# Performance work log

Hardware: AMD Instinct MI355X
Metric: run time of the kernel (lower is better)

## Reference

```python
import jax, jax.numpy as jnp
import numpy as np

B, NA, NB, D, NH, APO = 32, 128, 128, 512, 16, 128
VA, VB, SUP_BDIST = 64, 32, 8
INV_SQRT_2PI_FACT = (2.0 * np.pi) ** 0.5


def setup_inputs() -> dict:
    key = jax.random.key(0)
    ks = jax.random.split(key, 20)
    atoms = jax.random.randint(ks[0], (B, NA), 0, VA)
    chirals = jax.random.randint(ks[1], (B, NA), 0, 4)
    coordinates = jax.random.normal(ks[2], (B, NA, 3), dtype=jnp.float32) * 5.0
    bonds = jax.random.randint(ks[3], (B, NA, NA), 0, VB)
    i0 = jax.random.randint(ks[4], (B, NB), 0, NA)
    off = jax.random.randint(ks[5], (B, NB), 1, NA)
    i1 = (i0 + off) % NA  # guarantee distinct endpoints so one-hot sum <= 1
    bond_indices = jnp.stack([i0, i1], axis=-1)
    bond_values = jax.random.randint(ks[6], (B, NB), 0, VB)
    bdist = jax.random.randint(ks[7], (B, NA, NA), 0, SUP_BDIST)
    sc = 0.02
    # embedding tables; rows for padding_idx=0 zeroed like torch nn.Embedding
    atype_emb = (jax.random.normal(ks[8], (VA, D)) * sc).at[0].set(0.0)
    chiral_emb = (jax.random.normal(ks[9], (4, D)) * sc).at[0].set(0.0)
    apair_w_tab = jax.random.normal(ks[10], (VA * VA, APO)) * sc
    apair_b_tab = jax.random.normal(ks[11], (VA * VA, APO)) * sc
    means = jax.random.normal(ks[12], (APO,)) * 0.1
    stds = jnp.ones((APO,), jnp.float32) + jax.random.normal(ks[13], (APO,)) * 0.1
    bond_emb_tab = (jax.random.normal(ks[14], (VB, NH)) * sc).at[0].set(0.0)
    lin_W = jax.random.normal(ks[15], (APO, NH)) * (1.0 / np.sqrt(APO))
    lin_b = jax.random.normal(ks[16], (NH,)) * sc
    btype_tab = (jax.random.normal(ks[17], (VB, D)) * sc).at[0].set(0.0)
    bond_atom_tab = (jax.random.normal(ks[18], (VA, D)) * sc).at[0].set(0.0)
    ab_connect_tab = (jax.random.normal(ks[19], (2, NH)) * sc).at[0].set(0.0)
    return dict(atoms=atoms, chirals=chirals, coordinates=coordinates, bonds=bonds,
                bond_indices=bond_indices, bond_values=bond_values, bdist=bdist,
                atype_emb=atype_emb, chiral_emb=chiral_emb, apair_w_tab=apair_w_tab,
                apair_b_tab=apair_b_tab, means=means, stds=stds, bond_emb_tab=bond_emb_tab,
                lin_W=lin_W, lin_b=lin_b, btype_tab=btype_tab, bond_atom_tab=bond_atom_tab,
                ab_connect_tab=ab_connect_tab)


def reference(atoms, chirals, coordinates, bonds, bond_indices, bond_values, bdist,
              atype_emb, chiral_emb, apair_w_tab, apair_b_tab, means, stds,
              bond_emb_tab, lin_W, lin_b, btype_tab, bond_atom_tab, ab_connect_tab):
    batch, n_atom = atoms.shape
    n_bond = bond_values.shape[1]
    # --- node embeddings ---
    atoms_e = atype_emb[atoms] + chiral_emb[chirals]                 # [B,Na,D]
    bonds_e = btype_tab[bond_values]                                  # [B,Nb,D]
    a0 = jnp.take_along_axis(atoms, bond_indices[:, :, 0], axis=1)    # [B,Nb]
    a1 = jnp.take_along_axis(atoms, bond_indices[:, :, 1], axis=1)
    bonds_e = bonds_e + bond_atom_tab[a0] + bond_atom_tab[a1]
    atoms_emb = jnp.concatenate([atoms_e, bonds_e], axis=1).transpose(1, 0, 2)  # [Na+Nb,B,D]
    # --- pairwise distances + RBF-modulated pair features ---
    diff = coordinates[:, None, :, :] - coordinates[:, :, None, :]    # [B,Na,Na,3]
    distances = jnp.sqrt(jnp.sum(diff * diff, axis=-1))               # [B,Na,Na]
    pair_idx = atoms[:, None, :] * VA + atoms[:, :, None]             # [B,Na,Na]
    x = apair_w_tab[pair_idx] * distances[..., None] + apair_b_tab[pair_idx]  # [B,Na,Na,APO]
    s = jnp.abs(stds) + 1e-5
    x = jnp.exp(-0.5 * jnp.square((x - means) / s)) / (INV_SQRT_2PI_FACT * s)
    apairs = jnp.einsum('bijp,ph->bijh', x, lin_W) + lin_b + bond_emb_tab[bonds]  # [B,Na,Na,NH]
    # --- atom-bond connectivity block ---
    oh = (jax.nn.one_hot(bond_indices[:, :, 0], n_atom, dtype=jnp.int32)
          + jax.nn.one_hot(bond_indices[:, :, 1], n_atom, dtype=jnp.int32))      # [B,Nb,Na]
    oh = oh * (bond_values != 0).astype(jnp.int32)[..., None]
    abpairs = ab_connect_tab[oh]                                       # [B,Nb,Na,NH]
    top = jnp.concatenate([apairs, abpairs], axis=1)                   # [B,Na+Nb,Na,NH]
    right = jnp.concatenate([abpairs.transpose(0, 2, 1, 3),
                             jnp.zeros((batch, n_bond, n_bond, NH), apairs.dtype)], axis=1)
    apairs = jnp.concatenate([top, right], axis=2)                     # [B,L,L,NH]
    padding_mask = jnp.concatenate([atoms == 0, bond_values == 0], axis=1)  # [B,L]
    apairs = jnp.where(padding_mask[:, None, :, None], -jnp.inf, apairs)
    apairs = apairs.transpose(0, 3, 1, 2)                              # [B,NH,L,L]
    # --- extended bdist ---
    oh_d = oh * SUP_BDIST
    bdist_out = jnp.concatenate([
        jnp.concatenate([bdist, oh_d], axis=1),
        jnp.concatenate([oh_d.transpose(0, 2, 1),
                         jnp.zeros((batch, n_bond, n_bond), oh_d.dtype)], axis=1)], axis=2)
    return atoms_emb, apairs, bdist_out, padding_mask
```

## Files before the change

kernel.cpp:

```cpp
#include <hip/hip_runtime.h>
#include <hip/hip_fp16.h>
#include <math.h>

#define B_ 32
#define NA_ 128
#define NB_ 128
#define D_ 512
#define NH_ 16
#define APO_ 128
#define L_ 256
#define VA_ 64

#define NEG_BIG (-3.0e38f)

#define WSB_WBT  2048
#define WSB_WBF  8192
#define WSB_BBF  (8192 + (1 << 20))
#define WS_NEED_BYTES (8192 + (2 << 20))

typedef __attribute__((ext_vector_type(8))) _Float16 f16x8;
typedef __attribute__((ext_vector_type(4))) float f32x4;

#define TROW 136

static __device__ __forceinline__ void nt_store(float* p, float v) {
    __builtin_nontemporal_store(v, p);
}
static __device__ __forceinline__ void nt_store2(float* p, float2 v) {
    __builtin_nontemporal_store(v.x, p);
    __builtin_nontemporal_store(v.y, p + 1);
}

__global__ __launch_bounds__(256) void k0_fold(
    const float* __restrict__ wtab, const float* __restrict__ btab,
    const float* __restrict__ means, const float* __restrict__ stds,
    const float* __restrict__ linW, char* __restrict__ wsb) {
    int t = blockIdx.x * 256 + threadIdx.x;
    int ai = t >> 13;
    int aj = (t >> 7) & 63;
    int p = t & (APO_ - 1);
    int src = (aj << 13) + (ai << 7) + p;
    float s = fabsf(stds[p]) + 1e-5f;
    float si = 1.0f / s;
    _Float16* wbf = (_Float16*)(wsb + WSB_WBF);
    _Float16* bbf = (_Float16*)(wsb + WSB_BBF);
    wbf[t] = (_Float16)(wtab[src] * si);
    bbf[t] = (_Float16)((btab[src] - means[p]) * si);
    if (blockIdx.x == 0) {
        _Float16* wbT = (_Float16*)(wsb + WSB_WBT);
        for (int q = threadIdx.x; q < NH_ * APO_; q += 256) {
            int h = q >> 7, pp = q & 127;
            float s2 = fabsf(stds[pp]) + 1e-5f;
            float cof = 0.39894228040143270f / s2;
            wbT[q] = (_Float16)(linW[pp * NH_ + h] * cof);
        }
    }
}

__global__ __launch_bounds__(256, 4) void k_mega(
    const int* __restrict__ atoms, const int* __restrict__ chirals,
    const float* __restrict__ coords, const int* __restrict__ bonds,
    const int* __restrict__ bond_idx, const int* __restrict__ bond_vals,
    const int* __restrict__ bdist,
    const float* __restrict__ atype, const float* __restrict__ chiral_t,
    const float* __restrict__ btype, const float* __restrict__ batom,
    const float* __restrict__ ab_tab, const float* __restrict__ linb,
    const float* __restrict__ bond_emb, const char* __restrict__ wsb,
    float* __restrict__ out0, float* __restrict__ out1,
    float* __restrict__ out2, float* __restrict__ out3) {
    __shared__ _Float16 tab[2][64 * TROW];
    float (*epi)[129] = (float (*)[129]) & tab[0][0];

    int b = blockIdx.x >> 8;
    int r = blockIdx.x & 255;
    int tid = threadIdx.x;

    if (r < NA_) {
        int i = r;
        int wave = tid >> 6;
        int lane = tid & 63;
        int col = lane & 15;
        int kg = lane >> 4;

        int ai = atoms[b * NA_ + i];

        const _Float16* gw = (const _Float16*)(wsb + WSB_WBF) + (size_t)ai * (64 * APO_);
        const _Float16* gb = (const _Float16*)(wsb + WSB_BBF) + (size_t)ai * (64 * APO_);
#pragma unroll
        for (int it = 0; it < 4; ++it) {
            int g = (it * 256 + tid) * 8;
            int row = g >> 7, off = g & 127;
            *(f16x8*)&tab[0][row * TROW + off] = *(const f16x8*)(gw + g);
            *(f16x8*)&tab[1][row * TROW + off] = *(const f16x8*)(gb + g);
        }

        int j2 = tid & 127;
        int hg = tid >> 7;
        int ajr2 = atoms[b * NA_ + j2];
        int bij2 = bonds[((size_t)b * NA_ + i) * NA_ + j2];
        const float4* ber4 = (const float4*)(bond_emb + (size_t)bij2 * NH_);
        float4 berA = ber4[hg * 2 + 0];
        float4 berB = ber4[hg * 2 + 1];

        float cx = coords[((size_t)b * NA_ + i) * 3 + 0];
        float cy = coords[((size_t)b * NA_ + i) * 3 + 1];
        float cz = coords[((size_t)b * NA_ + i) * 3 + 2];
        __half2 d2[2];
        int rowh[2];
#pragma unroll
        for (int tt = 0; tt < 2; ++tt) {
            int jA = (wave * 2 + tt) * 16 + col;
            int ajt = atoms[b * NA_ + jA];
            float dx = coords[((size_t)b * NA_ + jA) * 3 + 0] - cx;
            float dy = coords[((size_t)b * NA_ + jA) * 3 + 1] - cy;
            float dz = coords[((size_t)b * NA_ + jA) * 3 + 2] - cz;
            float dist = sqrtf(dx * dx + dy * dy + dz * dz);
            d2[tt] = __float2half2_rn(dist);
            rowh[tt] = ajt * TROW;
        }

        const _Float16* wbT = (const _Float16*)(wsb + WSB_WBT);
        f16x8 Bf[4];
#pragma unroll
        for (int ks = 0; ks < 4; ++ks)
            Bf[ks] = *(const f16x8*)(wbT + col * APO_ + ks * 32 + kg * 8);

        const __half2 KE2 = __float2half2_rn(-0.72134752044448170f);

        __syncthreads();

        f32x4 accv[2];
#pragma unroll
        for (int tt = 0; tt < 2; ++tt) {
            f32x4 acc = {0.f, 0.f, 0.f, 0.f};
#pragma unroll
            for (int ks = 0; ks < 4; ++ks) {
                f16x8 w8 = *(const f16x8*)&tab[0][rowh[tt] + ks * 32 + kg * 8];
                f16x8 b8 = *(const f16x8*)&tab[1][rowh[tt] + ks * 32 + kg * 8];
                const __half2* wh = (const __half2*)&w8;
                const __half2* bh = (const __half2*)&b8;
                f16x8 af;
                __half2* eh = (__half2*)&af;
#pragma unroll
                for (int q = 0; q < 4; ++q) {
                    __half2 xh = __hfma2(wh[q], d2[tt], bh[q]);
                    __half2 t2 = __hmul2(__hmul2(xh, xh), KE2);
                    eh[q] = h2exp2(t2);
                }
                acc = __builtin_amdgcn_mfma_f32_16x16x32_f16(af, Bf[ks], acc, 0, 0, 0);
            }
            accv[tt] = acc;
        }
        __syncthreads();

#pragma unroll
        for (int tt = 0; tt < 2; ++tt) {
            int jb = (wave * 2 + tt) * 16;
#pragma unroll
            for (int rr = 0; rr < 4; ++rr)
                epi[col][jb + kg * 4 + rr] = accv[tt][rr];
        }
        __syncthreads();

        float berx[8] = {berA.x, berA.y, berA.z, berA.w, berB.x, berB.y, berB.z, berB.w};
        bool maskj = (ajr2 == 0);
        float* opb = out1 + (size_t)b * NH_ * L_ * L_ + (size_t)(hg * 8) * (L_ * L_)
                   + (size_t)i * L_ + j2;
#pragma unroll
        for (int q = 0; q < 8; ++q) {
            int h = hg * 8 + q;
            float v = epi[h][j2] + linb[h] + berx[q];
            nt_store(opb + (size_t)q * (L_ * L_), maskj ? NEG_BIG : v);
        }
    }

    int c = tid;

    {
        float2 v;
        if (r < NA_) {
            int a = atoms[b * NA_ + r];
            int ch = chirals[b * NA_ + r];
            float2 v1 = ((const float2*)(atype + (size_t)a * D_))[c];
            float2 v2 = ((const float2*)(chiral_t + (size_t)ch * D_))[c];
            v = make_float2(v1.x + v2.x, v1.y + v2.y);
        } else {
            int k = r - NA_;
            int bv = bond_vals[b * NB_ + k];
            int i0 = bond_idx[(b * NB_ + k) * 2 + 0];
            int i1 = bond_idx[(b * NB_ + k) * 2 + 1];
            int a0 = atoms[b * NA_ + i0];
            int a1 = atoms[b * NA_ + i1];
            float2 v1 = ((const float2*)(btype + (size_t)bv * D_))[c];
            float2 v2 = ((const float2*)(batom + (size_t)a0 * D_))[c];
            float2 v3 = ((const float2*)(batom + (size_t)a1 * D_))[c];
            v = make_float2(v1.x + v2.x + v3.x, v1.y + v2.y + v3.y);
        }
        nt_store2(out0 + ((size_t)r * B_ + b) * D_ + 2 * c, v);
    }

    {
        float v = 0.0f;
        if (r < NA_) {
            if (c < NA_) {
                v = (float)bdist[((size_t)b * NA_ + r) * NA_ + c];
            } else {
                int k = c - NA_;
                int bv = bond_vals[b * NB_ + k];
                int i0 = bond_idx[(b * NB_ + k) * 2 + 0];
                int i1 = bond_idx[(b * NB_ + k) * 2 + 1];
                v = (bv != 0 && (i0 == r || i1 == r)) ? 8.0f : 0.0f;
            }
        } else if (c < NA_) {
            int k = r - NA_;
            int bv = bond_vals[b * NB_ + k];
            int i0 = bond_idx[(b * NB_ + k) * 2 + 0];
            int i1 = bond_idx[(b * NB_ + k) * 2 + 1];
            v = (bv != 0 && (i0 == c || i1 == c)) ? 8.0f : 0.0f;
        }
        nt_store(out2 + ((size_t)b * L_ + r) * L_ + c, v);
    }

    if (r == 0) {
        bool m = (c < NA_) ? (atoms[b * NA_ + c] == 0)
                           : (bond_vals[b * NB_ + (c - NA_)] == 0);
        nt_store(out3 + b * L_ + c, m ? 1.0f : 0.0f);
    }

    if (r >= NA_ || c >= NA_) {
        float ohv = 0.0f;
        bool mask;
        if (c < NA_) {
            int k = r - NA_;
            int bv = bond_vals[b * NB_ + k];
            int i0 = bond_idx[(b * NB_ + k) * 2 + 0];
            int i1 = bond_idx[(b * NB_ + k) * 2 + 1];
            ohv = (bv != 0 && (i0 == c || i1 == c)) ? 1.0f : 0.0f;
            mask = (atoms[b * NA_ + c] == 0);
        } else {
            int k = c - NA_;
            int bv = bond_vals[b * NB_ + k];
            mask = (bv == 0);
            if (r < NA_) {
                int i0 = bond_idx[(b * NB_ + k) * 2 + 0];
                int i1 = bond_idx[(b * NB_ + k) * 2 + 1];
                ohv = (bv != 0 && (i0 == r || i1 == r)) ? 1.0f : 0.0f;
            }
        }
        float* op = out1 + (size_t)b * NH_ * L_ * L_ + (size_t)r * L_ + c;
#pragma unroll
        for (int h = 0; h < NH_; ++h) {
            float v = mask ? NEG_BIG : ohv * ab_tab[NH_ + h];
            nt_store(op + (size_t)h * (L_ * L_), v);
        }
    }
}

__global__ __launch_bounds__(128) void k2_pair(
    const int* __restrict__ atoms, const float* __restrict__ coords,
    const int* __restrict__ bonds, const float* __restrict__ wtab,
    const float* __restrict__ btab, const float* __restrict__ linW,
    const float* __restrict__ linb, const float* __restrict__ bond_emb,
    const float* __restrict__ means, const float* __restrict__ stds,
    float* __restrict__ out1) {
    int b = blockIdx.x >> 7;
    int i = blockIdx.x & (NA_ - 1);
    int j = threadIdx.x;
    int ai = atoms[b * NA_ + i];
    int aj = atoms[b * NA_ + j];
    float cx = coords[((size_t)b * NA_ + i) * 3 + 0];
    float cy = coords[((size_t)b * NA_ + i) * 3 + 1];
    float cz = coords[((size_t)b * NA_ + i) * 3 + 2];
    float dx = coords[((size_t)b * NA_ + j) * 3 + 0] - cx;
    float dy = coords[((size_t)b * NA_ + j) * 3 + 1] - cy;
    float dz = coords[((size_t)b * NA_ + j) * 3 + 2] - cz;
    float dist = sqrtf(dx * dx + dy * dy + dz * dz);
    int idx = aj * VA_ + ai;
    const float4* wrow = (const float4*)(wtab + (size_t)idx * APO_);
    const float4* brow = (const float4*)(btab + (size_t)idx * APO_);
    float acc[NH_];
#pragma unroll
    for (int h = 0; h < NH_; ++h) acc[h] = 0.0f;
    const float KE = -0.72134752044448170f;
    for (int pp = 0; pp < APO_ / 4; ++pp) {
        float4 w4 = wrow[pp];
        float4 b4 = brow[pp];
        const float* wq = (const float*)&w4;
        const float* bq = (const float*)&b4;
#pragma unroll
        for (int q = 0; q < 4; ++q) {
            int p = pp * 4 + q;
            float s = fabsf(stds[p]) + 1e-5f;
            float si = 1.0f / s;
            float xh = fmaf(wq[q] * si, dist, fmaf(bq[q], si, -means[p] * si));
            float g = si * 0.39894228040143270f * exp2f(KE * xh * xh);
            const float* Wr = linW + p * NH_;
#pragma unroll
            for (int h = 0; h < NH_; ++h) acc[h] = fmaf(g, Wr[h], acc[h]);
        }
    }
    int bij = bonds[((size_t)b * NA_ + i) * NA_ + j];
    bool maskj = (aj == 0);
    float* op = out1 + (size_t)b * NH_ * L_ * L_ + (size_t)i * L_ + j;
#pragma unroll
    for (int h = 0; h < NH_; ++h) {
        float v = acc[h] + linb[h] + bond_emb[(size_t)bij * NH_ + h];
        op[(size_t)h * (L_ * L_)] = maskj ? NEG_BIG : v;
    }
}

__global__ __launch_bounds__(256) void k_fill(
    const int* __restrict__ atoms, const int* __restrict__ chirals,
    const int* __restrict__ bond_idx, const int* __restrict__ bond_vals,
    const int* __restrict__ bdist,
    const float* __restrict__ atype, const float* __restrict__ chiral_t,
    const float* __restrict__ btype, const float* __restrict__ batom,
    const float* __restrict__ ab_tab,
    float* __restrict__ out0, float* __restrict__ out1,
    float* __restrict__ out2, float* __restrict__ out3) {
    int b = blockIdx.x >> 8;
    int r = blockIdx.x & 255;
    int c = threadIdx.x;
    {
        float2 v;
        if (r < NA_) {
            int a = atoms[b * NA_ + r];
            int ch = chirals[b * NA_ + r];
            float2 v1 = ((const float2*)(atype + (size_t)a * D_))[c];
            float2 v2 = ((const float2*)(chiral_t + (size_t)ch * D_))[c];
            v = make_float2(v1.x + v2.x, v1.y + v2.y);
        } else {
            int k = r - NA_;
            int bv = bond_vals[b * NB_ + k];
            int i0 = bond_idx[(b * NB_ + k) * 2 + 0];
            int i1 = bond_idx[(b * NB_ + k) * 2 + 1];
            int a0 = atoms[b * NA_ + i0];
            int a1 = atoms[b * NA_ + i1];
            float2 v1 = ((const float2*)(btype + (size_t)bv * D_))[c];
            float2 v2 = ((const float2*)(batom + (size_t)a0 * D_))[c];
            float2 v3 = ((const float2*)(batom + (size_t)a1 * D_))[c];
            v = make_float2(v1.x + v2.x + v3.x, v1.y + v2.y + v3.y);
        }
        ((float2*)(out0 + ((size_t)r * B_ + b) * D_))[c] = v;
    }
    {
        float v = 0.0f;
        if (r < NA_) {
            if (c < NA_) {
                v = (float)bdist[((size_t)b * NA_ + r) * NA_ + c];
            } else {
                int k = c - NA_;
                int bv = bond_vals[b * NB_ + k];
                int i0 = bond_idx[(b * NB_ + k) * 2 + 0];
                int i1 = bond_idx[(b * NB_ + k) * 2 + 1];
                v = (bv != 0 && (i0 == r || i1 == r)) ? 8.0f : 0.0f;
            }
        } else if (c < NA_) {
            int k = r - NA_;
            int bv = bond_vals[b * NB_ + k];
            int i0 = bond_idx[(b * NB_ + k) * 2 + 0];
            int i1 = bond_idx[(b * NB_ + k) * 2 + 1];
            v = (bv != 0 && (i0 == c || i1 == c)) ? 8.0f : 0.0f;
        }
        out2[((size_t)b * L_ + r) * L_ + c] = v;
    }
    if (r == 0) {
        bool m = (c < NA_) ? (atoms[b * NA_ + c] == 0)
                           : (bond_vals[b * NB_ + (c - NA_)] == 0);
        out3[b * L_ + c] = m ? 1.0f : 0.0f;
    }
    if (r >= NA_ || c >= NA_) {
        float ohv = 0.0f;
        bool mask;
        if (c < NA_) {
            int k = r - NA_;
            int bv = bond_vals[b * NB_ + k];
            int i0 = bond_idx[(b * NB_ + k) * 2 + 0];
            int i1 = bond_idx[(b * NB_ + k) * 2 + 1];
            ohv = (bv != 0 && (i0 == c || i1 == c)) ? 1.0f : 0.0f;
            mask = (atoms[b * NA_ + c] == 0);
        } else {
            int k = c - NA_;
            int bv = bond_vals[b * NB_ + k];
            mask = (bv == 0);
            if (r < NA_) {
                int i0 = bond_idx[(b * NB_ + k) * 2 + 0];
                int i1 = bond_idx[(b * NB_ + k) * 2 + 1];
                ohv = (bv != 0 && (i0 == r || i1 == r)) ? 1.0f : 0.0f;
            }
        }
        float* op = out1 + (size_t)b * NH_ * L_ * L_ + (size_t)r * L_ + c;
#pragma unroll
        for (int h = 0; h < NH_; ++h) {
            float v = mask ? NEG_BIG : ohv * ab_tab[NH_ + h];
            op[(size_t)h * (L_ * L_)] = v;
        }
    }
}

extern "C" void kernel_launch(void* const* d_in, const int* in_sizes, int n_in,
                              void* d_out, int out_size, void* d_ws, size_t ws_size,
                              hipStream_t stream) {
    const int*   atoms     = (const int*)d_in[0];
    const int*   chirals   = (const int*)d_in[1];
    const float* coords    = (const float*)d_in[2];
    const int*   bonds     = (const int*)d_in[3];
    const int*   bond_idx  = (const int*)d_in[4];
    const int*   bond_vals = (const int*)d_in[5];
    const int*   bdist     = (const int*)d_in[6];
    const float* atype     = (const float*)d_in[7];
    const float* chiral_t  = (const float*)d_in[8];
    const float* wtab      = (const float*)d_in[9];
    const float* btab      = (const float*)d_in[10];
    const float* means     = (const float*)d_in[11];
    const float* stds      = (const float*)d_in[12];
    const float* bond_emb  = (const float*)d_in[13];
    const float* linW      = (const float*)d_in[14];
    const float* linb      = (const float*)d_in[15];
    const float* btype     = (const float*)d_in[16];
    const float* batom     = (const float*)d_in[17];
    const float* ab_tab    = (const float*)d_in[18];

    float* out  = (float*)d_out;
    float* out0 = out;
    float* out1 = out0 + (size_t)L_ * B_ * D_;
    float* out2 = out1 + (size_t)B_ * NH_ * L_ * L_;
    float* out3 = out2 + (size_t)B_ * L_ * L_;
    char*  wsb  = (char*)d_ws;

    bool use_fold = ws_size >= (size_t)WS_NEED_BYTES;

    if (use_fold) {
        hipLaunchKernelGGL(k0_fold, dim3(VA_ * VA_ * APO_ / 256), dim3(256), 0, stream,
                           wtab, btab, means, stds, linW, wsb);
        hipLaunchKernelGGL(k_mega, dim3(B_ * L_), dim3(256), 0, stream,
                           atoms, chirals, coords, bonds, bond_idx, bond_vals, bdist,
                           atype, chiral_t, btype, batom, ab_tab, linb, bond_emb, wsb,
                           out0, out1, out2, out3);
    } else {
        hipLaunchKernelGGL(k2_pair, dim3(B_ * NA_), dim3(NA_), 0, stream,
                           atoms, coords, bonds, wtab, btab, linW, linb, bond_emb,
                           means, stds, out1);
        hipLaunchKernelGGL(k_fill, dim3(B_ * L_), dim3(256), 0, stream,
                           atoms, chirals, bond_idx, bond_vals, bdist,
                           atype, chiral_t, btype, batom, ab_tab,
                           out0, out1, out2, out3);
    }
}
```

Measured before the change: 47.75 us.

## Sort atoms by type per batch to cluster LDS table row accesses

Adds a small kernel that counting-sorts each batch's atom indices by atom type into a workspace permutation. The pair kernel then processes j in sorted order, so lanes in a wave read the same or nearby LDS table rows, which is meant to cut bank conflicts and scattered reads. Results are scattered back to original positions in the epilogue. This costs an extra kernel launch, an indirect index load, and a larger workspace requirement; if the workspace is too small, the fallback path is taken instead.

```diff
diff --git a/kernel.cpp b/kernel.cpp
--- a/kernel.cpp
+++ b/kernel.cpp
@@ -16,7 +16,8 @@
 #define WSB_WBT  2048
 #define WSB_WBF  8192
 #define WSB_BBF  (8192 + (1 << 20))
-#define WS_NEED_BYTES (8192 + (2 << 20))
+#define WSB_PERM (8192 + (2 << 20))
+#define WS_NEED_BYTES (WSB_PERM + B_ * NA_ * 4)
 
 typedef __attribute__((ext_vector_type(8))) _Float16 f16x8;
 typedef __attribute__((ext_vector_type(4))) float f32x4;
@@ -57,6 +58,26 @@
     }
 }
 
+__global__ __launch_bounds__(128) void k0p_sort(
+    const int* __restrict__ atoms, char* __restrict__ wsb) {
+    __shared__ int cnt[VA_];
+    int b = blockIdx.x;
+    int tid = threadIdx.x;
+    int a = atoms[b * NA_ + tid];
+    if (tid < VA_) cnt[tid] = 0;
+    __syncthreads();
+    atomicAdd(&cnt[a], 1);
+    __syncthreads();
+    if (tid == 0) {
+        int run = 0;
+#pragma unroll
+        for (int v = 0; v < VA_; ++v) { int cc = cnt[v]; cnt[v] = run; run += cc; }
+    }
+    __syncthreads();
+    int slot = atomicAdd(&cnt[a], 1);
+    ((int*)(wsb + WSB_PERM))[b * NA_ + slot] = tid;
+}
+
 __global__ __launch_bounds__(256, 4) void k_mega(
     const int* __restrict__ atoms, const int* __restrict__ chirals,
     const float* __restrict__ coords, const int* __restrict__ bonds,
@@ -83,6 +104,7 @@
         int kg = lane >> 4;
 
         int ai = atoms[b * NA_ + i];
+        const int* permb = (const int*)(wsb + WSB_PERM) + b * NA_;
 
         const _Float16* gw = (const _Float16*)(wsb + WSB_WBF) + (size_t)ai * (64 * APO_);
         const _Float16* gb = (const _Float16*)(wsb + WSB_BBF) + (size_t)ai * (64 * APO_);
@@ -107,9 +129,11 @@
         float cz = coords[((size_t)b * NA_ + i) * 3 + 2];
         __half2 d2[2];
         int rowh[2];
+        int jApos[2];
 #pragma unroll
         for (int tt = 0; tt < 2; ++tt) {
-            int jA = (wave * 2 + tt) * 16 + col;
+            int jA = permb[(wave * 2 + tt) * 16 + col];
+            jApos[tt] = jA;
             int ajt = atoms[b * NA_ + jA];
             float dx = coords[((size_t)b * NA_ + jA) * 3 + 0] - cx;
             float dy = coords[((size_t)b * NA_ + jA) * 3 + 1] - cy;
@@ -118,6 +142,7 @@
             d2[tt] = __float2half2_rn(dist);
             rowh[tt] = ajt * TROW;
         }
+        (void)jApos;
 
         const _Float16* wbT = (const _Float16*)(wsb + WSB_WBT);
         f16x8 Bf[4];
@@ -158,7 +183,7 @@
             int jb = (wave * 2 + tt) * 16;
 #pragma unroll
             for (int rr = 0; rr < 4; ++rr)
-                epi[col][jb + kg * 4 + rr] = accv[tt][rr];
+                epi[col][permb[jb + kg * 4 + rr]] = accv[tt][rr];
         }
         __syncthreads();
 
@@ -433,6 +458,7 @@
     if (use_fold) {
         hipLaunchKernelGGL(k0_fold, dim3(VA_ * VA_ * APO_ / 256), dim3(256), 0, stream,
                            wtab, btab, means, stds, linW, wsb);
+        hipLaunchKernelGGL(k0p_sort, dim3(B_), dim3(NA_), 0, stream, atoms, wsb);
         hipLaunchKernelGGL(k_mega, dim3(B_ * L_), dim3(256), 0, stream,
                            atoms, chirals, coords, bonds, bond_idx, bond_vals, bdist,
                            atype, chiral_t, btype, batom, ab_tab, linb, bond_emb, wsb,
```

Measured after the change: 53.17 us. 11.4% more time.
